# Optimization experiments

Hardware: AMD Instinct MI355X
Metric: run time of the kernel (lower is better)

Reference implementation:

```python
import jax, jax.numpy as jnp
import numpy as np

N = 100000   # nodes
E = 1600000  # edges
EPS = 1e-5   # BatchNorm eps

def setup_inputs() -> dict:
    key = jax.random.key(0)
    ks = jax.random.split(key, 18)
    x = jax.random.normal(ks[0], (N, 128), jnp.float32)
    edge_index = jax.random.randint(ks[1], (2, E), 0, N, dtype=jnp.int64)
    # GCN layer weights (Glorot-ish scale) and biases
    W1 = jax.random.normal(ks[2], (128, 64), jnp.float32) * 0.1
    b1 = jnp.zeros((64,), jnp.float32)
    W2 = jax.random.normal(ks[3], (64, 64), jnp.float32) * 0.1
    b2 = jnp.zeros((64,), jnp.float32)
    W3 = jax.random.normal(ks[4], (64, 16), jnp.float32) * 0.1
    b3 = jnp.zeros((16,), jnp.float32)
    # BatchNorm (eval mode) affine params + running stats, 2 BN layers of width 64
    g1 = jax.random.uniform(ks[5], (64,), jnp.float32, 0.5, 1.5)
    be1 = jax.random.normal(ks[6], (64,), jnp.float32) * 0.1
    m1 = jax.random.normal(ks[7], (64,), jnp.float32) * 0.1
    v1 = jax.random.uniform(ks[8], (64,), jnp.float32, 0.5, 1.5)
    g2 = jax.random.uniform(ks[9], (64,), jnp.float32, 0.5, 1.5)
    be2 = jax.random.normal(ks[10], (64,), jnp.float32) * 0.1
    m2 = jax.random.normal(ks[11], (64,), jnp.float32) * 0.1
    v2 = jax.random.uniform(ks[12], (64,), jnp.float32, 0.5, 1.5)
    return {"x": x, "edge_index": edge_index,
            "W1": W1, "b1": b1, "W2": W2, "b2": b2, "W3": W3, "b3": b3,
            "g1": g1, "be1": be1, "m1": m1, "v1": v1,
            "g2": g2, "be2": be2, "m2": m2, "v2": v2}

def _gcn_graph(edge_index):
    # add self-loops, compute symmetric normalization deg^-1/2 * deg^-1/2
    loop = jnp.arange(N, dtype=edge_index.dtype)
    src = jnp.concatenate([edge_index[0], loop])
    dst = jnp.concatenate([edge_index[1], loop])
    deg = jax.ops.segment_sum(jnp.ones_like(dst, dtype=jnp.float32), dst, num_segments=N)
    dinv = jnp.where(deg > 0, jax.lax.rsqrt(jnp.maximum(deg, 1.0)), 0.0)
    norm = dinv[src] * dinv[dst]  # [E+N]
    return src, dst, norm

def reference(x, edge_index, W1, b1, W2, b2, W3, b3,
              g1, be1, m1, v1, g2, be2, m2, v2):
    src, dst, norm = _gcn_graph(edge_index)

    def conv(h, W, b):
        h = h @ W                              # [N, d_out]
        msg = h[src] * norm[:, None]           # gather + scale, [E+N, d_out]
        return jax.ops.segment_sum(msg, dst, num_segments=N) + b

    def bn(h, g, be, m, v):
        return g * (h - m) * jax.lax.rsqrt(v + EPS) + be

    h = jax.nn.relu(bn(conv(x, W1, b1), g1, be1, m1, v1))
    h = jax.nn.relu(bn(conv(h, W2, b2), g2, be2, m2, v2))
    return jax.nn.sigmoid(conv(h, W3, b3))
```

## Files before the change

kernel.cpp:

```cpp
#include <hip/hip_runtime.h>
#include <math.h>

#define NN 100000
#define NE 1600000
#define EPSBN 1e-5f
#define NB_SCAN 391
#define NBUCK 391

static __device__ __forceinline__ unsigned short f2bf(float f) {
    unsigned int u = __float_as_uint(f);
    u += 0x7fffu + ((u >> 16) & 1u);
    return (unsigned short)(u >> 16);
}
static __device__ __forceinline__ float bf2f(unsigned short s) {
    return __uint_as_float(((unsigned int)s) << 16);
}
static __device__ __forceinline__ void fma4(float4& a, float s, const float4& w) {
    a.x = fmaf(s, w.x, a.x); a.y = fmaf(s, w.y, a.y);
    a.z = fmaf(s, w.z, a.z); a.w = fmaf(s, w.w, a.w);
}
static __device__ __forceinline__ void fma2(float2& a, float s, const float2& w) {
    a.x = fmaf(s, w.x, a.x); a.y = fmaf(s, w.y, a.y);
}

__global__ __launch_bounds__(256) void zero_cnt(int* __restrict__ cnt) {
    int i = blockIdx.x * 256 + threadIdx.x;
    if (i < NN) cnt[i] = 0;
}

__global__ __launch_bounds__(256) void hist_kernel(const int* __restrict__ dst,
                                                   int* __restrict__ cnt) {
    int e = blockIdx.x * 256 + threadIdx.x;
    if (e < NE) atomicAdd(&cnt[dst[e]], 1);
}

__global__ __launch_bounds__(256) void scan1(const int* __restrict__ cnt,
                                             int* __restrict__ rex,
                                             int* __restrict__ part) {
    __shared__ int sh[256];
    int t = threadIdx.x;
    int i = blockIdx.x * 256 + t;
    int val = (i < NN) ? cnt[i] : 0;
    sh[t] = val;
    __syncthreads();
    for (int off = 1; off < 256; off <<= 1) {
        int x = (t >= off) ? sh[t - off] : 0;
        __syncthreads();
        sh[t] += x;
        __syncthreads();
    }
    if (i < NN) rex[i] = sh[t] - val;
    if (t == 255) part[blockIdx.x] = sh[255];
}

__global__ __launch_bounds__(512) void scan2(const int* __restrict__ part,
                                             int* __restrict__ partoff) {
    __shared__ int sh[512];
    int t = threadIdx.x;
    int val = (t < NB_SCAN) ? part[t] : 0;
    sh[t] = val;
    __syncthreads();
    for (int off = 1; off < 512; off <<= 1) {
        int x = (t >= off) ? sh[t - off] : 0;
        __syncthreads();
        sh[t] += x;
        __syncthreads();
    }
    partoff[t] = sh[t] - val;
}

__global__ __launch_bounds__(256) void scan3(const int* __restrict__ rex,
                                             const int* __restrict__ partoff,
                                             const int* __restrict__ cnt,
                                             int* __restrict__ row_start,
                                             int* __restrict__ bcur,
                                             float* __restrict__ dinv) {
    int i = blockIdx.x * 256 + threadIdx.x;
    if (i < NN) {
        row_start[i] = rex[i] + partoff[i >> 8];
        dinv[i] = rsqrtf(1.0f + (float)cnt[i]);
        if (i == 0) row_start[NN] = NE;
    }
    if (i < 512) bcur[i] = 0;
}

__global__ __launch_bounds__(256) void bin_kernel(const int* __restrict__ src,
                                                  const int* __restrict__ dst,
                                                  const int* __restrict__ bb0,
                                                  int* __restrict__ bcur,
                                                  unsigned int* __restrict__ bucketed) {
    __shared__ int lh[NBUCK];
    __shared__ int lbase[NBUCK];
    __shared__ int lcur[NBUCK];
    int t = threadIdx.x;
    for (int b = t; b < NBUCK; b += 256) lh[b] = 0;
    __syncthreads();
    int e0 = blockIdx.x * 4096;
#pragma unroll
    for (int i = 0; i < 16; ++i) {
        int e = e0 + i * 256 + t;
        if (e < NE) atomicAdd(&lh[dst[e] >> 8], 1);
    }
    __syncthreads();
    for (int b = t; b < NBUCK; b += 256) {
        lbase[b] = bb0[b] + atomicAdd(&bcur[b], lh[b]);
        lcur[b] = 0;
    }
    __syncthreads();
#pragma unroll
    for (int i = 0; i < 16; ++i) {
        int e = e0 + i * 256 + t;
        if (e < NE) {
            int d = dst[e], s = src[e];
            int b = d >> 8;
            int pos = lbase[b] + atomicAdd(&lcur[b], 1);
            bucketed[pos] = (unsigned int)s | ((unsigned int)(d & 255) << 24);
        }
    }
}

__global__ __launch_bounds__(256) void fine_scatter(const unsigned int* __restrict__ bucketed,
                                                    const int* __restrict__ bb0,
                                                    const int* __restrict__ row_start,
                                                    int* __restrict__ sorted_src) {
    __shared__ int lcur[256];
    int b = blockIdx.x;
    int t = threadIdx.x;
    lcur[t] = 0;
    __syncthreads();
    int e0 = bb0[b], e1 = bb0[b + 1];
    for (int e = e0 + t; e < e1; e += 256) {
        unsigned int p = bucketed[e];
        int dl = (int)(p >> 24);
        int s  = (int)(p & 0xFFFFFFu);
        int pos = row_start[b * 256 + dl] + atomicAdd(&lcur[dl], 1);
        sorted_src[pos] = s;
    }
}

__global__ __launch_bounds__(256) void gemm_128_64_v3(const float* __restrict__ x,
                                                      const float* __restrict__ W,
                                                      const float* __restrict__ dinv,
                                                      unsigned short* __restrict__ hs) {
    __shared__ float xs[64][132];
    __shared__ float ws[128][64];
    int tid = threadIdx.x;
    int bn = blockIdx.x * 64;
    for (int id = tid; id < 2048; id += 256) {
        int r = id >> 4, c4 = id & 15;
        *(float4*)&ws[r][c4 * 4] = *(const float4*)(W + r * 64 + c4 * 4);
    }
    for (int id = tid; id < 64 * 33; id += 256) {
        int r = id / 33, c4 = id - r * 33;
        int n = bn + r; if (n >= NN) n = NN - 1;
        float4 v = make_float4(0.f, 0.f, 0.f, 0.f);
        if (c4 < 32) v = *(const float4*)(x + (size_t)n * 128 + c4 * 4);
        *(float4*)&xs[r][c4 * 4] = v;
    }
    __syncthreads();
    int tn = tid >> 4, tf = tid & 15;
    int f0 = tf * 4;
    float4 acc[4] = {{0,0,0,0},{0,0,0,0},{0,0,0,0},{0,0,0,0}};
#pragma unroll 2
    for (int k = 0; k < 128; k += 4) {
        float4 w0 = *(const float4*)&ws[k + 0][f0];
        float4 w1 = *(const float4*)&ws[k + 1][f0];
        float4 w2 = *(const float4*)&ws[k + 2][f0];
        float4 w3 = *(const float4*)&ws[k + 3][f0];
#pragma unroll
        for (int i = 0; i < 4; ++i) {
            float4 xa = *(const float4*)&xs[tn * 4 + i][k];
            fma4(acc[i], xa.x, w0); fma4(acc[i], xa.y, w1);
            fma4(acc[i], xa.z, w2); fma4(acc[i], xa.w, w3);
        }
    }
#pragma unroll
    for (int i = 0; i < 4; ++i) {
        int n = bn + tn * 4 + i;
        if (n < NN) {
            float di = dinv[n];
            ushort4 u;
            u.x = f2bf(acc[i].x * di); u.y = f2bf(acc[i].y * di);
            u.z = f2bf(acc[i].z * di); u.w = f2bf(acc[i].w * di);
            *(ushort4*)(hs + (size_t)n * 64 + f0) = u;
        }
    }
}

__global__ __launch_bounds__(256) void gemm_64_64_v3(const float* __restrict__ x,
                                                     const float* __restrict__ W,
                                                     const float* __restrict__ dinv,
                                                     unsigned short* __restrict__ hs) {
    __shared__ float xs[64][68];
    __shared__ float ws[64][64];
    int tid = threadIdx.x;
    int bn = blockIdx.x * 64;
    for (int id = tid; id < 1024; id += 256) {
        int r = id >> 4, c4 = id & 15;
        *(float4*)&ws[r][c4 * 4] = *(const float4*)(W + r * 64 + c4 * 4);
    }
    for (int id = tid; id < 64 * 17; id += 256) {
        int r = id / 17, c4 = id - r * 17;
        int n = bn + r; if (n >= NN) n = NN - 1;
        float4 v = make_float4(0.f, 0.f, 0.f, 0.f);
        if (c4 < 16) v = *(const float4*)(x + (size_t)n * 64 + c4 * 4);
        *(float4*)&xs[r][c4 * 4] = v;
    }
    __syncthreads();
    int tn = tid >> 4, tf = tid & 15;
    int f0 = tf * 4;
    float4 acc[4] = {{0,0,0,0},{0,0,0,0},{0,0,0,0},{0,0,0,0}};
#pragma unroll 2
    for (int k = 0; k < 64; k += 4) {
        float4 w0 = *(const float4*)&ws[k + 0][f0];
        float4 w1 = *(const float4*)&ws[k + 1][f0];
        float4 w2 = *(const float4*)&ws[k + 2][f0];
        float4 w3 = *(const float4*)&ws[k + 3][f0];
#pragma unroll
        for (int i = 0; i < 4; ++i) {
            float4 xa = *(const float4*)&xs[tn * 4 + i][k];
            fma4(acc[i], xa.x, w0); fma4(acc[i], xa.y, w1);
            fma4(acc[i], xa.z, w2); fma4(acc[i], xa.w, w3);
        }
    }
#pragma unroll
    for (int i = 0; i < 4; ++i) {
        int n = bn + tn * 4 + i;
        if (n < NN) {
            float di = dinv[n];
            ushort4 u;
            u.x = f2bf(acc[i].x * di); u.y = f2bf(acc[i].y * di);
            u.z = f2bf(acc[i].z * di); u.w = f2bf(acc[i].w * di);
            *(ushort4*)(hs + (size_t)n * 64 + f0) = u;
        }
    }
}

__global__ __launch_bounds__(256) void gemm_64_16_v3(const float* __restrict__ x,
                                                     const float* __restrict__ W,
                                                     const float* __restrict__ dinv,
                                                     unsigned short* __restrict__ hs) {
    __shared__ float xs[128][68];
    __shared__ float ws[64][16];
    int tid = threadIdx.x;
    int bn = blockIdx.x * 128;
    for (int id = tid; id < 256; id += 256) {
        int r = id >> 2, c4 = id & 3;
        *(float4*)&ws[r][c4 * 4] = *(const float4*)(W + r * 16 + c4 * 4);
    }
    for (int id = tid; id < 128 * 17; id += 256) {
        int r = id / 17, c4 = id - r * 17;
        int n = bn + r; if (n >= NN) n = NN - 1;
        float4 v = make_float4(0.f, 0.f, 0.f, 0.f);
        if (c4 < 16) v = *(const float4*)(x + (size_t)n * 64 + c4 * 4);
        *(float4*)&xs[r][c4 * 4] = v;
    }
    __syncthreads();
    int tn = tid >> 3, tf = tid & 7;
    int f0 = tf * 2;
    float2 acc[4] = {{0,0},{0,0},{0,0},{0,0}};
#pragma unroll 2
    for (int k = 0; k < 64; k += 4) {
        float2 w0 = *(const float2*)&ws[k + 0][f0];
        float2 w1 = *(const float2*)&ws[k + 1][f0];
        float2 w2 = *(const float2*)&ws[k + 2][f0];
        float2 w3 = *(const float2*)&ws[k + 3][f0];
#pragma unroll
        for (int i = 0; i < 4; ++i) {
            float4 xa = *(const float4*)&xs[tn * 4 + i][k];
            fma2(acc[i], xa.x, w0); fma2(acc[i], xa.y, w1);
            fma2(acc[i], xa.z, w2); fma2(acc[i], xa.w, w3);
        }
    }
#pragma unroll
    for (int i = 0; i < 4; ++i) {
        int n = bn + tn * 4 + i;
        if (n < NN) {
            float di = dinv[n];
            ushort2 u;
            u.x = f2bf(acc[i].x * di); u.y = f2bf(acc[i].y * di);
            *(ushort2*)(hs + (size_t)n * 16 + f0) = u;
        }
    }
}

__global__ __launch_bounds__(256) void csr_agg64_bn_relu(const int* __restrict__ rs,
                                                         const int* __restrict__ ss,
                                                         const unsigned short* __restrict__ hs,
                                                         const float* __restrict__ dinv,
                                                         const float* __restrict__ b,
                                                         const float* __restrict__ g,
                                                         const float* __restrict__ be,
                                                         const float* __restrict__ m,
                                                         const float* __restrict__ v,
                                                         float* __restrict__ out) {
    int lane = threadIdx.x & 63;
    int r = blockIdx.x * 4 + (threadIdx.x >> 6);
    int e0 = rs[r], e1 = rs[r + 1];
    float a0 = bf2f(hs[(size_t)r * 64 + lane]);
    float a1 = 0.f, a2 = 0.f, a3 = 0.f;
    for (int base = e0; base < e1; base += 64) {
        int nb = e1 - base; if (nb > 64) nb = 64;
        int sidx = (lane < nb) ? ss[base + lane] : 0;
        int j = 0;
        for (; j + 4 <= nb; j += 4) {
            int s0 = __shfl(sidx, j),     s1 = __shfl(sidx, j + 1);
            int s2 = __shfl(sidx, j + 2), s3 = __shfl(sidx, j + 3);
            a0 += bf2f(hs[(size_t)s0 * 64 + lane]);
            a1 += bf2f(hs[(size_t)s1 * 64 + lane]);
            a2 += bf2f(hs[(size_t)s2 * 64 + lane]);
            a3 += bf2f(hs[(size_t)s3 * 64 + lane]);
        }
        for (; j < nb; ++j)
            a0 += bf2f(hs[(size_t)__shfl(sidx, j) * 64 + lane]);
    }
    float acc = (a0 + a1) + (a2 + a3);
    float h = dinv[r] * acc + b[lane];
    h = g[lane] * (h - m[lane]) * rsqrtf(v[lane] + EPSBN) + be[lane];
    out[(size_t)r * 64 + lane] = fmaxf(h, 0.f);
}

__global__ __launch_bounds__(256) void csr_agg16_sigmoid(const int* __restrict__ rs,
                                                         const int* __restrict__ ss,
                                                         const unsigned short* __restrict__ hs,
                                                         const float* __restrict__ dinv,
                                                         const float* __restrict__ b,
                                                         float* __restrict__ out) {
    int lane = threadIdx.x & 63;
    int wid = blockIdx.x * 4 + (threadIdx.x >> 6);
    int grp = lane >> 4, fl = lane & 15;
    int r = wid * 4 + grp;
    int e0 = rs[r], e1 = rs[r + 1];
    float a0 = bf2f(hs[(size_t)r * 16 + fl]);
    float a1 = 0.f, a2 = 0.f, a3 = 0.f;
    for (int base = e0; base < e1; base += 16) {
        int nb = e1 - base; if (nb > 16) nb = 16;
        int sidx = (fl < nb) ? ss[base + fl] : 0;
        int j = 0;
        for (; j + 4 <= nb; j += 4) {
            int s0 = __shfl(sidx, grp * 16 + j),     s1 = __shfl(sidx, grp * 16 + j + 1);
            int s2 = __shfl(sidx, grp * 16 + j + 2), s3 = __shfl(sidx, grp * 16 + j + 3);
            a0 += bf2f(hs[(size_t)s0 * 16 + fl]);
            a1 += bf2f(hs[(size_t)s1 * 16 + fl]);
            a2 += bf2f(hs[(size_t)s2 * 16 + fl]);
            a3 += bf2f(hs[(size_t)s3 * 16 + fl]);
        }
        for (; j < nb; ++j)
            a0 += bf2f(hs[(size_t)__shfl(sidx, grp * 16 + j) * 16 + fl]);
    }
    float acc = (a0 + a1) + (a2 + a3);
    float h = dinv[r] * acc + b[fl];
    out[(size_t)r * 16 + fl] = 1.0f / (1.0f + expf(-h));
}

extern "C" void kernel_launch(void* const* d_in, const int* in_sizes, int n_in,
                              void* d_out, int out_size, void* d_ws, size_t ws_size,
                              hipStream_t stream) {
    const float* x   = (const float*)d_in[0];
    const int*   ei  = (const int*)d_in[1];
    const float* W1  = (const float*)d_in[2];
    const float* b1  = (const float*)d_in[3];
    const float* W2  = (const float*)d_in[4];
    const float* b2  = (const float*)d_in[5];
    const float* W3  = (const float*)d_in[6];
    const float* b3  = (const float*)d_in[7];
    const float* g1  = (const float*)d_in[8];
    const float* be1 = (const float*)d_in[9];
    const float* m1  = (const float*)d_in[10];
    const float* v1  = (const float*)d_in[11];
    const float* g2  = (const float*)d_in[12];
    const float* be2 = (const float*)d_in[13];
    const float* m2  = (const float*)d_in[14];
    const float* v2  = (const float*)d_in[15];
    float* out = (float*)d_out;

    const int* srcp = ei;
    const int* dstp = ei + NE;

    float* dinv = (float*)d_ws;
    float* A    = dinv + NN;
    unsigned short* Bh = (unsigned short*)(A + (size_t)NN * 64);
    int* cnt        = (int*)(Bh + (size_t)NN * 64);
    int* rex        = cnt + NN;
    int* row_start  = rex + NN;
    int* bcur       = row_start + NN + 2;
    int* part       = bcur + 512;
    int* partoff    = part + 512;
    int* sorted_src = partoff + 512;
    unsigned int* bucketed = (unsigned int*)(sorted_src + NE);

    dim3 blk(256);
    int gN    = (NN + 255) / 256;
    int gE    = (NE + 255) / 256;
    int gBIN  = (NE + 4095) / 4096;
    int gG1   = (NN + 63) / 64;
    int gG3   = (NN + 127) / 128;
    int gA64  = NN / 4;
    int gA16  = NN / 16;

    zero_cnt<<<gN, blk, 0, stream>>>(cnt);
    hist_kernel<<<gE, blk, 0, stream>>>(dstp, cnt);
    scan1<<<gN, blk, 0, stream>>>(cnt, rex, part);
    scan2<<<1, 512, 0, stream>>>(part, partoff);
    scan3<<<gN, blk, 0, stream>>>(rex, partoff, cnt, row_start, bcur, dinv);
    bin_kernel<<<gBIN, blk, 0, stream>>>(srcp, dstp, partoff, bcur, bucketed);
    fine_scatter<<<NBUCK, blk, 0, stream>>>(bucketed, partoff, row_start, sorted_src);

    gemm_128_64_v3<<<gG1, blk, 0, stream>>>(x, W1, dinv, Bh);
    csr_agg64_bn_relu<<<gA64, blk, 0, stream>>>(row_start, sorted_src, Bh, dinv,
                                                b1, g1, be1, m1, v1, A);
    gemm_64_64_v3<<<gG1, blk, 0, stream>>>(A, W2, dinv, Bh);
    csr_agg64_bn_relu<<<gA64, blk, 0, stream>>>(row_start, sorted_src, Bh, dinv,
                                                b2, g2, be2, m2, v2, A);
    gemm_64_16_v3<<<gG3, blk, 0, stream>>>(A, W3, dinv, Bh);
    csr_agg16_sigmoid<<<gA16, blk, 0, stream>>>(row_start, sorted_src, Bh, dinv, b3, out);
}
```

Before: 416.6 us.

## Replace per-node histogram and three-pass scan with bucket counts and in-block scan

The CSR build no longer computes a global per-node degree histogram with atomics and a three-kernel scan. It counts edges per 256-node bucket using shared-memory histograms, scans the 391 bucket totals, and then has the fine scatter kernel build each bucket's per-node histogram, scan it locally, and write row_start and dinv itself. This cuts global atomics on 100k counters, two full-size kernel passes and several launches, in exchange for the fine scatter reading its bucket twice.

```diff
diff --git a/kernel.cpp b/kernel.cpp
--- a/kernel.cpp
+++ b/kernel.cpp
@@ -4,7 +4,6 @@
 #define NN 100000
 #define NE 1600000
 #define EPSBN 1e-5f
-#define NB_SCAN 391
 #define NBUCK 391
 
 static __device__ __forceinline__ unsigned short f2bf(float f) {
@@ -23,41 +22,35 @@
     a.x = fmaf(s, w.x, a.x); a.y = fmaf(s, w.y, a.y);
 }
 
-__global__ __launch_bounds__(256) void zero_cnt(int* __restrict__ cnt) {
-    int i = blockIdx.x * 256 + threadIdx.x;
-    if (i < NN) cnt[i] = 0;
-}
-
-__global__ __launch_bounds__(256) void hist_kernel(const int* __restrict__ dst,
-                                                   int* __restrict__ cnt) {
-    int e = blockIdx.x * 256 + threadIdx.x;
-    if (e < NE) atomicAdd(&cnt[dst[e]], 1);
-}
-
-__global__ __launch_bounds__(256) void scan1(const int* __restrict__ cnt,
-                                             int* __restrict__ rex,
-                                             int* __restrict__ part) {
-    __shared__ int sh[256];
+__global__ __launch_bounds__(512) void init_small(int* __restrict__ bkcnt,
+                                                  int* __restrict__ bcur) {
     int t = threadIdx.x;
-    int i = blockIdx.x * 256 + t;
-    int val = (i < NN) ? cnt[i] : 0;
-    sh[t] = val;
-    __syncthreads();
-    for (int off = 1; off < 256; off <<= 1) {
-        int x = (t >= off) ? sh[t - off] : 0;
-        __syncthreads();
-        sh[t] += x;
-        __syncthreads();
-    }
-    if (i < NN) rex[i] = sh[t] - val;
-    if (t == 255) part[blockIdx.x] = sh[255];
-}
-
-__global__ __launch_bounds__(512) void scan2(const int* __restrict__ part,
-                                             int* __restrict__ partoff) {
+    bkcnt[t] = 0;
+    bcur[t] = 0;
+}
+
+__global__ __launch_bounds__(256) void bucket_count(const int* __restrict__ dst,
+                                                    int* __restrict__ bkcnt) {
+    __shared__ int lh[NBUCK];
+    int t = threadIdx.x;
+    for (int b = t; b < NBUCK; b += 256) lh[b] = 0;
+    __syncthreads();
+    int e0 = blockIdx.x * 4096;
+#pragma unroll
+    for (int i = 0; i < 16; ++i) {
+        int e = e0 + i * 256 + t;
+        if (e < NE) atomicAdd(&lh[dst[e] >> 8], 1);
+    }
+    __syncthreads();
+    for (int b = t; b < NBUCK; b += 256)
+        if (lh[b]) atomicAdd(&bkcnt[b], lh[b]);
+}
+
+__global__ __launch_bounds__(512) void scan2(const int* __restrict__ bkcnt,
+                                             int* __restrict__ bb0) {
     __shared__ int sh[512];
     int t = threadIdx.x;
-    int val = (t < NB_SCAN) ? part[t] : 0;
+    int val = (t < NBUCK) ? bkcnt[t] : 0;
     sh[t] = val;
     __syncthreads();
     for (int off = 1; off < 512; off <<= 1) {
@@ -66,22 +59,7 @@
         sh[t] += x;
         __syncthreads();
     }
-    partoff[t] = sh[t] - val;
-}
-
-__global__ __launch_bounds__(256) void scan3(const int* __restrict__ rex,
-                                             const int* __restrict__ partoff,
-                                             const int* __restrict__ cnt,
-                                             int* __restrict__ row_start,
-                                             int* __restrict__ bcur,
-                                             float* __restrict__ dinv) {
-    int i = blockIdx.x * 256 + threadIdx.x;
-    if (i < NN) {
-        row_start[i] = rex[i] + partoff[i >> 8];
-        dinv[i] = rsqrtf(1.0f + (float)cnt[i]);
-        if (i == 0) row_start[NN] = NE;
-    }
-    if (i < 512) bcur[i] = 0;
+    bb0[t] = sh[t] - val;
 }
 
 __global__ __launch_bounds__(256) void bin_kernel(const int* __restrict__ src,
@@ -119,22 +97,45 @@
     }
 }
 
-__global__ __launch_bounds__(256) void fine_scatter(const unsigned int* __restrict__ bucketed,
-                                                    const int* __restrict__ bb0,
-                                                    const int* __restrict__ row_start,
-                                                    int* __restrict__ sorted_src) {
+__global__ __launch_bounds__(256) void fine_scatter_fused(const unsigned int* __restrict__ bucketed,
+                                                          const int* __restrict__ bb0,
+                                                          int* __restrict__ row_start,
+                                                          float* __restrict__ dinv,
+                                                          int* __restrict__ sorted_src) {
+    __shared__ int hist[256];
+    __shared__ int sc[256];
+    __shared__ int rsl[256];
     __shared__ int lcur[256];
-    int b = blockIdx.x;
-    int t = threadIdx.x;
-    lcur[t] = 0;
+    int b = blockIdx.x, t = threadIdx.x;
+    hist[t] = 0; lcur[t] = 0;
     __syncthreads();
     int e0 = bb0[b], e1 = bb0[b + 1];
+    for (int e = e0 + t; e < e1; e += 256)
+        atomicAdd(&hist[bucketed[e] >> 24], 1);
+    __syncthreads();
+    int val = hist[t];
+    sc[t] = val;
+    __syncthreads();
+    for (int off = 1; off < 256; off <<= 1) {
+        int x = (t >= off) ? sc[t - off] : 0;
+        __syncthreads();
+        sc[t] += x;
+        __syncthreads();
+    }
+    int ex = sc[t] - val;
+    int node = b * 256 + t;
+    if (node < NN) {
+        row_start[node] = e0 + ex;
+        dinv[node] = rsqrtf(1.0f + (float)val);
+    }
+    if (node == NN) row_start[NN] = NE;
+    rsl[t] = e0 + ex;
+    __syncthreads();
     for (int e = e0 + t; e < e1; e += 256) {
         unsigned int p = bucketed[e];
         int dl = (int)(p >> 24);
-        int s  = (int)(p & 0xFFFFFFu);
-        int pos = row_start[b * 256 + dl] + atomicAdd(&lcur[dl], 1);
-        sorted_src[pos] = s;
+        int pos = rsl[dl] + atomicAdd(&lcur[dl], 1);
+        sorted_src[pos] = (int)(p & 0xFFFFFFu);
     }
 }
 
@@ -380,31 +381,25 @@
     float* dinv = (float*)d_ws;
     float* A    = dinv + NN;
     unsigned short* Bh = (unsigned short*)(A + (size_t)NN * 64);
-    int* cnt        = (int*)(Bh + (size_t)NN * 64);
-    int* rex        = cnt + NN;
-    int* row_start  = rex + NN;
-    int* bcur       = row_start + NN + 2;
-    int* part       = bcur + 512;
-    int* partoff    = part + 512;
-    int* sorted_src = partoff + 512;
+    int* row_start  = (int*)(Bh + (size_t)NN * 64);
+    int* bkcnt      = row_start + NN + 2;
+    int* bb0        = bkcnt + 512;
+    int* bcur       = bb0 + 512;
+    int* sorted_src = bcur + 512;
     unsigned int* bucketed = (unsigned int*)(sorted_src + NE);
 
     dim3 blk(256);
-    int gN    = (NN + 255) / 256;
-    int gE    = (NE + 255) / 256;
     int gBIN  = (NE + 4095) / 4096;
     int gG1   = (NN + 63) / 64;
     int gG3   = (NN + 127) / 128;
     int gA64  = NN / 4;
     int gA16  = NN / 16;
 
-    zero_cnt<<<gN, blk, 0, stream>>>(cnt);
-    hist_kernel<<<gE, blk, 0, stream>>>(dstp, cnt);
-    scan1<<<gN, blk, 0, stream>>>(cnt, rex, part);
-    scan2<<<1, 512, 0, stream>>>(part, partoff);
-    scan3<<<gN, blk, 0, stream>>>(rex, partoff, cnt, row_start, bcur, dinv);
-    bin_kernel<<<gBIN, blk, 0, stream>>>(srcp, dstp, partoff, bcur, bucketed);
-    fine_scatter<<<NBUCK, blk, 0, stream>>>(bucketed, partoff, row_start, sorted_src);
+    init_small<<<1, 512, 0, stream>>>(bkcnt, bcur);
+    bucket_count<<<gBIN, blk, 0, stream>>>(dstp, bkcnt);
+    scan2<<<1, 512, 0, stream>>>(bkcnt, bb0);
+    bin_kernel<<<gBIN, blk, 0, stream>>>(srcp, dstp, bb0, bcur, bucketed);
+    fine_scatter_fused<<<NBUCK, blk, 0, stream>>>(bucketed, bb0, row_start, dinv, sorted_src);
 
     gemm_128_64_v3<<<gG1, blk, 0, stream>>>(x, W1, dinv, Bh);
     csr_agg64_bn_relu<<<gA64, blk, 0, stream>>>(row_start, sorted_src, Bh, dinv,
```

After: 361.1 us. -13.3%, faster.
